# Optimization experiments

Measured on AMD Instinct MI355X. Metric: run time of the kernel, lower is better.

Reference implementation:

```python
import jax, jax.numpy as jnp
import numpy as np

N_BINS = 20  # matches ECELoss_DRL(n_bins=20)


def setup_inputs() -> dict:
    key = jax.random.key(0)
    k1, k2 = jax.random.split(key)
    N, C = 1_000_000, 128
    logits = jax.random.normal(k1, (N, C), dtype=jnp.float32)
    softmaxes = jax.nn.softmax(logits, axis=-1)  # valid probabilities in (0,1]
    labels = jax.random.randint(k2, (N,), 0, C, dtype=jnp.int32)
    return {"softmaxes": softmaxes, "labels": labels}


def reference(softmaxes, labels):
    # torch.max(softmaxes, 1) -> (confidences, predictions)
    conf = jnp.max(softmaxes, axis=1)                  # [N]
    pred = jnp.argmax(softmaxes, axis=1)               # [N]
    acc = (pred == labels).astype(jnp.float32)         # [N]
    n = softmaxes.shape[0]

    # Bin b covers (b/n_bins, (b+1)/n_bins] -> single-pass bucketize replacing
    # the 20-iteration python loop of gt/le masks.
    bin_idx = jnp.clip(jnp.ceil(conf * N_BINS).astype(jnp.int32) - 1, 0, N_BINS - 1)

    ones = jnp.ones_like(conf)
    counts = jax.ops.segment_sum(ones, bin_idx, num_segments=N_BINS)    # [20]
    conf_sum = jax.ops.segment_sum(conf, bin_idx, num_segments=N_BINS)  # [20]
    acc_sum = jax.ops.segment_sum(acc, bin_idx, num_segments=N_BINS)    # [20]

    nonempty = counts > 0
    safe = jnp.maximum(counts, 1.0)
    avg_conf = conf_sum / safe
    avg_acc = acc_sum / safe
    prop = counts / n  # prop_in_bin = in_bin.float().mean()

    ece = jnp.sum(jnp.where(nonempty, jnp.abs(avg_conf - avg_acc) * prop, 0.0)).reshape(1)
    ys = jnp.where(nonempty, avg_acc, 0.0)  # per-bin accuracies, 0 for empty bins
    return ece, ys
```

## Files before the change

kernel.cpp:

```cpp
#include <hip/hip_runtime.h>

#define NBINS 20
#define C 128


__global__ __launch_bounds__(256) void ece_pass1(
    const float* __restrict__ sm, const int* __restrict__ labels, int N,
    double* __restrict__ g_csum, unsigned* __restrict__ g_cnt,
    unsigned* __restrict__ g_cor) {
  __shared__ float s_csum[NBINS];
  __shared__ unsigned s_cnt[NBINS];
  __shared__ unsigned s_cor[NBINS];
  const int tid = threadIdx.x;
  if (tid < NBINS) { s_csum[tid] = 0.f; s_cnt[tid] = 0u; s_cor[tid] = 0u; }
  __syncthreads();

  const int lane = tid & 63;
  const int wave = tid >> 6;
  const int sub  = lane >> 5;
  const int sl   = lane & 31;
  const long long gw    = (long long)blockIdx.x * 4 + wave;
  const long long waves = (long long)gridDim.x * 4;

  for (long long base = gw * 2; base < N; base += waves * 2) {
    const long long row = base + sub;
    float bestv = -1.f;
    int   besti = 0;
    if (row < N) {
      const float4 v = *(const float4*)(sm + row * (long long)C + sl * 4);
      bestv = v.x; besti = sl * 4;
      if (v.y > bestv) { bestv = v.y; besti = sl * 4 + 1; }
      if (v.z > bestv) { bestv = v.z; besti = sl * 4 + 2; }
      if (v.w > bestv) { bestv = v.w; besti = sl * 4 + 3; }
    }
#pragma unroll
    for (int off = 16; off >= 1; off >>= 1) {
      const float ov = __shfl_xor(bestv, off);
      const int   oi = __shfl_xor(besti, off);
      if (ov > bestv || (ov == bestv && oi < besti)) { bestv = ov; besti = oi; }
    }
    if (sl == 0 && row < N) {
      int bin = (int)ceilf(bestv * 20.0f) - 1;
      bin = min(max(bin, 0), NBINS - 1);
      const unsigned correct = (besti == labels[row]) ? 1u : 0u;
      atomicAdd(&s_csum[bin], bestv);
      atomicAdd(&s_cnt[bin], 1u);
      if (correct) atomicAdd(&s_cor[bin], 1u);
    }
  }
  __syncthreads();
  if (tid < NBINS && s_cnt[tid]) {
    atomicAdd(&g_cnt[tid], s_cnt[tid]);
    atomicAdd(&g_cor[tid], s_cor[tid]);
    atomicAdd(&g_csum[tid], (double)s_csum[tid]);
  }
}

__global__ void ece_pass2(const double* __restrict__ g_csum,
                          const unsigned* __restrict__ g_cnt,
                          const unsigned* __restrict__ g_cor,
                          float* __restrict__ out, int N) {
  const int i = threadIdx.x;
  double contrib = 0.0;
  if (i < NBINS) {
    const unsigned c = g_cnt[i];
    const double safe = c ? (double)c : 1.0;
    const double avg_conf = g_csum[i] / safe;
    const double avg_acc  = (double)g_cor[i] / safe;
    out[1 + i] = c ? (float)avg_acc : 0.f;
    if (c) contrib = fabs(avg_conf - avg_acc) * ((double)c / (double)N);
  }
#pragma unroll
  for (int off = 16; off >= 1; off >>= 1) contrib += __shfl_down(contrib, off);
  if (i == 0) out[0] = (float)contrib;
}

extern "C" void kernel_launch(void* const* d_in, const int* in_sizes, int n_in,
                              void* d_out, int out_size, void* d_ws, size_t ws_size,
                              hipStream_t stream) {
  const float* sm     = (const float*)d_in[0];
  const int*   labels = (const int*)d_in[1];
  const int N = in_sizes[1];

  double*   g_csum = (double*)d_ws;
  unsigned* g_cnt  = (unsigned*)((char*)d_ws + NBINS * sizeof(double));
  unsigned* g_cor  = g_cnt + NBINS;

  hipMemsetAsync(d_ws, 0, NBINS * sizeof(double) + 2 * NBINS * sizeof(unsigned),
                 stream);

  ece_pass1<<<2048, 256, 0, stream>>>(sm, labels, N, g_csum, g_cnt, g_cor);
  ece_pass2<<<1, 64, 0, stream>>>(g_csum, g_cnt, g_cor, (float*)d_out, N);
}
```

Measured before the change: 665.4 us.

## Process 16 rows per wave with 8 lanes per row and batched loads

Each wave now covers 16 rows per iteration: 8 lanes per row, each loading four float4 values, and two row groups are issued before any compute. This raises the number of loads in flight per thread and shortens the shuffle reduction from five steps to three. The cost is more registers per thread. Also, lanes in a row group read 128B-strided chunks per load instruction rather than one fully contiguous row segment.

```diff
diff --git a/kernel.cpp b/kernel.cpp
--- a/kernel.cpp
+++ b/kernel.cpp
@@ -16,36 +16,53 @@
   __syncthreads();
 
   const int lane = tid & 63;
-  const int wave = tid >> 6;
-  const int sub  = lane >> 5;
-  const int sl   = lane & 31;
-  const long long gw    = (long long)blockIdx.x * 4 + wave;
-  const long long waves = (long long)gridDim.x * 4;
+  const int p = lane & 7;
+  const int r = lane >> 3;
+  const long long gw     = (long long)blockIdx.x * 4 + (tid >> 6);
+  const long long stride = (long long)gridDim.x * 4 * 16;
 
-  for (long long base = gw * 2; base < N; base += waves * 2) {
-    const long long row = base + sub;
-    float bestv = -1.f;
-    int   besti = 0;
-    if (row < N) {
-      const float4 v = *(const float4*)(sm + row * (long long)C + sl * 4);
-      bestv = v.x; besti = sl * 4;
-      if (v.y > bestv) { bestv = v.y; besti = sl * 4 + 1; }
-      if (v.z > bestv) { bestv = v.z; besti = sl * 4 + 2; }
-      if (v.w > bestv) { bestv = v.w; besti = sl * 4 + 3; }
+  for (long long base = gw * 16; base < N; base += stride) {
+    float4 v[2][4];
+#pragma unroll
+    for (int g = 0; g < 2; ++g) {
+      const long long row = base + g * 8 + r;
+      if (row < N) {
+        const float4* rp = (const float4*)(sm + row * (long long)C);
+#pragma unroll
+        for (int k = 0; k < 4; ++k) v[g][k] = rp[p + k * 8];
+      } else {
+#pragma unroll
+        for (int k = 0; k < 4; ++k) v[g][k] = make_float4(-2.f, -2.f, -2.f, -2.f);
+      }
     }
+
 #pragma unroll
-    for (int off = 16; off >= 1; off >>= 1) {
-      const float ov = __shfl_xor(bestv, off);
-      const int   oi = __shfl_xor(besti, off);
-      if (ov > bestv || (ov == bestv && oi < besti)) { bestv = ov; besti = oi; }
-    }
-    if (sl == 0 && row < N) {
-      int bin = (int)ceilf(bestv * 20.0f) - 1;
-      bin = min(max(bin, 0), NBINS - 1);
-      const unsigned correct = (besti == labels[row]) ? 1u : 0u;
-      atomicAdd(&s_csum[bin], bestv);
-      atomicAdd(&s_cnt[bin], 1u);
-      if (correct) atomicAdd(&s_cor[bin], 1u);
+    for (int g = 0; g < 2; ++g) {
+      float bv = -3.f;
+      int bi = 0;
+#pragma unroll
+      for (int k = 0; k < 4; ++k) {
+        const float4 q = v[g][k];
+        const int b0 = k * 32 + p * 4;
+        if (q.x > bv) { bv = q.x; bi = b0; }
+        if (q.y > bv) { bv = q.y; bi = b0 + 1; }
+        if (q.z > bv) { bv = q.z; bi = b0 + 2; }
+        if (q.w > bv) { bv = q.w; bi = b0 + 3; }
+      }
+#pragma unroll
+      for (int off = 1; off <= 4; off <<= 1) {
+        const float ov = __shfl_xor(bv, off);
+        const int   oi = __shfl_xor(bi, off);
+        if (ov > bv || (ov == bv && oi < bi)) { bv = ov; bi = oi; }
+      }
+      const long long row = base + g * 8 + r;
+      if (p == 0 && row < N) {
+        int bin = (int)ceilf(bv * 20.0f) - 1;
+        bin = min(max(bin, 0), NBINS - 1);
+        atomicAdd(&s_csum[bin], bv);
+        atomicAdd(&s_cnt[bin], 1u);
+        if (bi == labels[row]) atomicAdd(&s_cor[bin], 1u);
+      }
     }
   }
   __syncthreads();
```

Result: no change. 655.5 us (-1.5%).
